# Kernel optimization log

Hardware: AMD Instinct MI355X
Metric: run time of the kernel (lower is better)

Reference implementation:

```python
import jax, jax.numpy as jnp
import numpy as np

EPS = 0.1
P, C, T_MLP, C_MLP, B = 196, 768, 384, 3072, 64


def yat(x, W, b, alpha):
    # x: (..., in), W: (out, in), b: (out,), alpha: (1,)
    dot_nb = jnp.einsum('...i,oi->...o', x, W)          # no-bias dot (shared GEMM)
    dot = dot_nb + b
    w_norm_sq = jnp.sum(W * W, axis=1)                   # (out,)
    x_norm_sq = jnp.sum(x * x, axis=-1, keepdims=True)   # (..., 1)
    dist_sq = w_norm_sq + x_norm_sq - 2.0 * dot_nb
    out_f = W.shape[0]
    scale_base = out_f / np.log(out_f + 1.0)
    scale = jnp.sqrt(jnp.asarray(scale_base, x.dtype)) ** alpha[0]
    return scale * (dot * dot) / (dist_sq + EPS)


def setup_inputs() -> dict:
    key = jax.random.key(0)
    ks = jax.random.split(key, 7)
    x = jax.random.normal(ks[0], (B, P, C), dtype=jnp.float32)
    # token-mixing YAT: in=P, out=T_MLP
    tw = jax.random.normal(ks[1], (T_MLP, P), dtype=jnp.float32) / np.sqrt(P)
    tb = jnp.zeros((T_MLP,), jnp.float32)
    t_alpha = jnp.ones((1,), jnp.float32)
    # token-mixing linear: T_MLP -> P
    w2 = jax.random.uniform(ks[2], (P, T_MLP), jnp.float32, -1, 1) / np.sqrt(T_MLP)
    b2 = jax.random.uniform(ks[3], (P,), jnp.float32, -1, 1) / np.sqrt(T_MLP)
    # channel-mixing YAT: in=C, out=C_MLP
    cw = jax.random.normal(ks[4], (C_MLP, C), dtype=jnp.float32) / np.sqrt(C)
    cb = jnp.zeros((C_MLP,), jnp.float32)
    c_alpha = jnp.ones((1,), jnp.float32)
    # channel-mixing linear: C_MLP -> C
    w4 = jax.random.uniform(ks[5], (C, C_MLP), jnp.float32, -1, 1) / np.sqrt(C_MLP)
    b4 = jax.random.uniform(ks[6], (C,), jnp.float32, -1, 1) / np.sqrt(C_MLP)
    return {"x": x, "tw": tw, "tb": tb, "t_alpha": t_alpha, "w2": w2, "b2": b2,
            "cw": cw, "cb": cb, "c_alpha": c_alpha, "w4": w4, "b4": b4}


def reference(x, tw, tb, t_alpha, w2, b2, cw, cb, c_alpha, w4, b4):
    # Token mixing (operates over patch dim)
    shortcut = x
    xt = jnp.swapaxes(x, 1, 2)                 # (B, C, P)
    h = yat(xt, tw, tb, t_alpha)               # (B, C, T_MLP)
    h = jnp.einsum('bct,pt->bcp', h, w2) + b2  # (B, C, P)
    x = shortcut + jnp.swapaxes(h, 1, 2)
    # Channel mixing (operates over hidden dim)
    shortcut = x
    h = yat(x, cw, cb, c_alpha)                # (B, P, C_MLP)
    h = jnp.einsum('bpm,cm->bpc', h, w4) + b4  # (B, P, C)
    return shortcut + h
```

## Files before the change

kernel.cpp:

```cpp
#include <hip/hip_runtime.h>
#include <hip/hip_bf16.h>
#include <math.h>

#define B_   64
#define P_   196
#define PPAD 224
#define C_   768
#define TM_  384
#define CM_  3072
#define EPSY 0.1f

typedef unsigned short u16;
typedef __attribute__((ext_vector_type(8))) short bf16x8;
typedef __attribute__((ext_vector_type(4))) float f32x4;

__device__ __forceinline__ float bf2f(u16 v) {
    return __uint_as_float(((unsigned int)v) << 16);
}
__device__ __forceinline__ u16 f2bf(float f) {
    unsigned int u = __float_as_uint(f);
    unsigned int rounding = 0x7FFFu + ((u >> 16) & 1u);
    return (u16)((u + rounding) >> 16);
}

__device__ __forceinline__ void gl_lds16(const u16* g, u16* l) {
    __builtin_amdgcn_global_load_lds(
        (const __attribute__((address_space(1))) unsigned int*)g,
        (__attribute__((address_space(3))) unsigned int*)l,
        16, 0, 0);
}


__global__ __launch_bounds__(256) void k_prep_xT(const float* __restrict__ x,
                                                 u16* __restrict__ xT,
                                                 float* __restrict__ xn1) {
    __shared__ u16 tile[32][33];
    __shared__ float colsum[32];
    const int b = blockIdx.z, p0 = blockIdx.x * 32, c0 = blockIdx.y * 32;
    const int tx = threadIdx.x & 31, ty = threadIdx.x >> 5;
    if (threadIdx.x < 32) colsum[threadIdx.x] = 0.f;
    const float* xb = x + (size_t)b * P_ * C_;
    float s = 0.f;
    #pragma unroll
    for (int r = 0; r < 4; ++r) {
        int p = p0 + ty + r * 8;
        float v = (p < P_) ? xb[(size_t)p * C_ + c0 + tx] : 0.f;
        u16 h = f2bf(v);
        tile[ty + r * 8][tx] = h;
        float vb = bf2f(h);
        s = fmaf(vb, vb, s);
    }
    __syncthreads();
    u16* dst = xT + ((size_t)b * C_ + c0) * PPAD + p0;
    #pragma unroll
    for (int r = 0; r < 4; ++r) {
        int cl = ty + r * 8;
        dst[(size_t)cl * PPAD + tx] = tile[tx][cl];
    }
    atomicAdd(&colsum[tx], s);
    __syncthreads();
    if (threadIdx.x < 32)
        atomicAdd(&xn1[(size_t)b * C_ + c0 + threadIdx.x], colsum[threadIdx.x]);
}

__device__ __forceinline__ void pad_norm_body(const float* in, u16* outb, float* norm,
                                              int rows, int inlen, int outlen,
                                              int bid, int tid) {
    int wave = (bid * 256 + tid) >> 6;
    int lane = tid & 63;
    if (wave >= rows) return;
    const float* src = in + (size_t)wave * inlen;
    u16* dst = outb + (size_t)wave * outlen;
    float s = 0.f;
    for (int i = lane; i < outlen; i += 64) {
        float v = (i < inlen) ? src[i] : 0.f;
        u16 h = f2bf(v);
        dst[i] = h;
        float vv = bf2f(h);
        s = fmaf(vv, vv, s);
    }
    #pragma unroll
    for (int off = 32; off > 0; off >>= 1) s += __shfl_down(s, off, 64);
    if (lane == 0) norm[wave] = s;
}

__global__ __launch_bounds__(256) void k_prep_weights(
    const float* __restrict__ tw, u16* __restrict__ twb, float* __restrict__ twn,
    const float* __restrict__ cw, u16* __restrict__ cwb, float* __restrict__ cwn,
    const float* __restrict__ w2, u16* __restrict__ w2b,
    const float* __restrict__ w4, u16* __restrict__ w4b) {
    int bid = blockIdx.x, tid = threadIdx.x;
    if (bid < 96) {
        pad_norm_body(tw, twb, twn, TM_, P_, PPAD, bid, tid);
    } else if (bid < 864) {
        pad_norm_body(cw, cwb, cwn, CM_, C_, C_, bid - 96, tid);
    } else if (bid < 1248) {
        int idx = (bid - 864) * 256 + tid;
        int row = idx / TM_;
        w2b[idx] = (row < P_) ? f2bf(w2[(size_t)row * TM_ + (idx % TM_)]) : (u16)0;
    } else {
        int idx = (bid - 1248) * 256 + tid;
        float4 v = ((const float4*)w4)[idx];
        ushort4 o;
        o.x = f2bf(v.x); o.y = f2bf(v.y); o.z = f2bf(v.z); o.w = f2bf(v.w);
        ((ushort4*)w4b)[idx] = o;
    }
}

__device__ __forceinline__ void mfma_mainloop(
    const u16* __restrict__ A, const u16* __restrict__ B,
    int lda, int ldb, int kiters,
    f32x4 (&acc)[4][4], u16* As, u16* Bs) {
    const int t = threadIdx.x;
    const int w = t >> 6, l = t & 63;
    const int quad = l >> 4, l15 = l & 15;
    const int row0 = t >> 2, kc = (t & 3) * 8;
    const int row1 = 64 + row0;

    gl_lds16(A + (size_t)row0 * lda + kc, As + w * 512);
    gl_lds16(A + (size_t)row1 * lda + kc, As + 2048 + w * 512);
    gl_lds16(B + (size_t)row0 * ldb + kc, Bs + w * 512);
    gl_lds16(B + (size_t)row1 * ldb + kc, Bs + 2048 + w * 512);
    __syncthreads();

    int cur = 0;
    for (int it = 0; it < kiters; ++it) {
        if (it + 1 < kiters) {
            const int k0 = (it + 1) * 32;
            const int nb = (cur ^ 1) * 4096;
            gl_lds16(A + (size_t)row0 * lda + k0 + kc, As + nb + w * 512);
            gl_lds16(A + (size_t)row1 * lda + k0 + kc, As + nb + 2048 + w * 512);
            gl_lds16(B + (size_t)row0 * ldb + k0 + kc, Bs + nb + w * 512);
            gl_lds16(B + (size_t)row1 * ldb + k0 + kc, Bs + nb + 2048 + w * 512);
        }
        const u16* Aw = As + cur * 4096 + (w >> 1) * 2048;
        const u16* Bw = Bs + cur * 4096 + (w & 1) * 2048;
        bf16x8 af[4], bfr[4];
        #pragma unroll
        for (int i = 0; i < 4; ++i)
            af[i] = *(const bf16x8*)(Aw + ((i * 16 + l15) * 32 + quad * 8));
        #pragma unroll
        for (int j = 0; j < 4; ++j)
            bfr[j] = *(const bf16x8*)(Bw + ((j * 16 + l15) * 32 + quad * 8));
        #pragma unroll
        for (int i = 0; i < 4; ++i)
            #pragma unroll
            for (int j = 0; j < 4; ++j)
                acc[i][j] = __builtin_amdgcn_mfma_f32_16x16x32_bf16(af[i], bfr[j], acc[i][j], 0, 0, 0);
        __syncthreads();
        cur ^= 1;
    }
}

#define MFMA_CORE(AP, BP, LDA, LDB, KITERS)                              \
    __shared__ u16 As[2 * 128 * 32];                                     \
    __shared__ u16 Bs[2 * 128 * 32];                                     \
    const int t = threadIdx.x;                                           \
    const int wid = t >> 6, lane = t & 63;                               \
    const int quad = lane >> 4, l15 = lane & 15;                         \
    f32x4 acc[4][4];                                                     \
    _Pragma("unroll")                                                    \
    for (int i = 0; i < 4; ++i)                                          \
        _Pragma("unroll")                                                \
        for (int j = 0; j < 4; ++j) acc[i][j] = (f32x4){0.f,0.f,0.f,0.f};\
    mfma_mainloop(AP, BP, LDA, LDB, KITERS, acc, As, Bs);                \
    const int rbase = m0 + (wid >> 1) * 64;                              \
    const int cbase = n0 + (wid & 1) * 64;

__global__ __launch_bounds__(256) void k1_token_yat(
    const u16* __restrict__ xT, const u16* __restrict__ twb,
    const float* __restrict__ tb, const float* __restrict__ twn,
    const float* __restrict__ xn1, const float* __restrict__ alpha, float sb,
    u16* __restrict__ h1) {
    const int m0 = (blockIdx.x + blockIdx.y * 8) * 128;
    const int n0 = blockIdx.z * 128;
    MFMA_CORE(xT + (size_t)m0 * PPAD, twb + (size_t)n0 * PPAD, PPAD, PPAD, PPAD / 32)
    float scale = powf(sqrtf(sb), alpha[0]);
    #pragma unroll
    for (int i = 0; i < 4; ++i) {
        #pragma unroll
        for (int j = 0; j < 4; ++j) {
            int col = cbase + j * 16 + l15;
            float bn = tb[col], wnn = twn[col];
            #pragma unroll
            for (int reg = 0; reg < 4; ++reg) {
                int row = rbase + i * 16 + quad * 4 + reg;
                float dnb = acc[i][j][reg];
                float dot = dnb + bn;
                float dist = wnn + xn1[row] - 2.f * dnb;
                h1[(size_t)row * TM_ + col] = f2bf(scale * dot * dot / (dist + EPSY));
            }
        }
    }
}

__global__ __launch_bounds__(256) void k3_chan_yat(
    const u16* __restrict__ x1b, const u16* __restrict__ cwb,
    const float* __restrict__ cb, const float* __restrict__ cwn,
    const float* __restrict__ xn2, const float* __restrict__ alpha, float sb,
    u16* __restrict__ h3) {
    const int mt = blockIdx.x + blockIdx.y * 8;
    if (mt >= B_ * P_ / 128) return;
    const int m0 = mt * 128;
    const int n0 = blockIdx.z * 128;
    MFMA_CORE(x1b + (size_t)m0 * C_, cwb + (size_t)n0 * C_, C_, C_, C_ / 32)
    float scale = powf(sqrtf(sb), alpha[0]);
    #pragma unroll
    for (int i = 0; i < 4; ++i) {
        #pragma unroll
        for (int j = 0; j < 4; ++j) {
            int col = cbase + j * 16 + l15;
            float bn = cb[col], wnn = cwn[col];
            #pragma unroll
            for (int reg = 0; reg < 4; ++reg) {
                int row = rbase + i * 16 + quad * 4 + reg;
                float dnb = acc[i][j][reg];
                float dot = dnb + bn;
                float dist = wnn + xn2[row] - 2.f * dnb;
                h3[(size_t)row * CM_ + col] = f2bf(scale * dot * dot / (dist + EPSY));
            }
        }
    }
}

__global__ __launch_bounds__(256) void k2_token_out(
    const u16* __restrict__ w2b, const u16* __restrict__ h1,
    const float* __restrict__ b2, const float* __restrict__ x,
    float* __restrict__ xn2, u16* __restrict__ x1b) {
    const int m0 = blockIdx.x * 128, n0 = blockIdx.y * 128;
    const u16* Bz = h1 + (size_t)blockIdx.z * C_ * TM_;
    MFMA_CORE(w2b + (size_t)m0 * TM_, Bz + (size_t)n0 * TM_, TM_, TM_, TM_ / 32)
    const float* rz = x + (size_t)blockIdx.z * P_ * C_;
    u16* oz = x1b + (size_t)blockIdx.z * P_ * C_;
    float* xrow = xn2 + (size_t)blockIdx.z * P_;
    #pragma unroll
    for (int i = 0; i < 4; ++i) {
        #pragma unroll
        for (int reg = 0; reg < 4; ++reg) {
            int row = rbase + i * 16 + quad * 4 + reg;
            if (row < P_) {
                float bm = b2[row];
                float s = 0.f;
                #pragma unroll
                for (int j = 0; j < 4; ++j) {
                    int col = cbase + j * 16 + l15;
                    float v = acc[i][j][reg] + bm + rz[(size_t)row * C_ + col];
                    u16 h = f2bf(v);
                    oz[(size_t)row * C_ + col] = h;
                    float vb = bf2f(h);
                    s = fmaf(vb, vb, s);
                }
                s += __shfl_xor(s, 1, 64);
                s += __shfl_xor(s, 2, 64);
                s += __shfl_xor(s, 4, 64);
                s += __shfl_xor(s, 8, 64);
                if (l15 == 0) atomicAdd(&xrow[row], s);
            }
        }
    }
}

__global__ __launch_bounds__(256) void k4_split(
    const u16* __restrict__ h3, const u16* __restrict__ w4b,
    u16* __restrict__ pbuf, int KK) {
    const int mt = blockIdx.x + blockIdx.y * 8;
    if (mt >= B_ * P_ / 128) return;
    const int m0 = mt * 128;
    const int nz = blockIdx.z;
    const int n0 = (nz % (C_ / 128)) * 128;
    const int ks = nz / (C_ / 128);
    const int kbase = ks * KK;
    MFMA_CORE(h3 + (size_t)m0 * CM_ + kbase, w4b + (size_t)n0 * CM_ + kbase,
              CM_, CM_, KK / 32)
    u16* dst = pbuf + (size_t)ks * ((size_t)B_ * P_ * C_);
    #pragma unroll
    for (int i = 0; i < 4; ++i) {
        #pragma unroll
        for (int j = 0; j < 4; ++j) {
            int col = cbase + j * 16 + l15;
            #pragma unroll
            for (int reg = 0; reg < 4; ++reg) {
                int row = rbase + i * 16 + quad * 4 + reg;
                dst[(size_t)row * C_ + col] = f2bf(acc[i][j][reg]);
            }
        }
    }
}

template <int NS>
__global__ __launch_bounds__(256) void k4_reduce(
    float* __restrict__ outp, const u16* __restrict__ pbuf,
    const u16* __restrict__ x1b, const float* __restrict__ b4) {
    int idx = blockIdx.x * 256 + threadIdx.x;
    int c = (idx * 4) % C_;
    ushort4 r = ((const ushort4*)x1b)[idx];
    float4 o;
    o.x = bf2f(r.x) + b4[c + 0];
    o.y = bf2f(r.y) + b4[c + 1];
    o.z = bf2f(r.z) + b4[c + 2];
    o.w = bf2f(r.w) + b4[c + 3];
    const size_t stride4 = (size_t)B_ * P_ * C_ / 4;
    #pragma unroll
    for (int s = 0; s < NS; ++s) {
        ushort4 p = ((const ushort4*)pbuf)[idx + s * stride4];
        o.x += bf2f(p.x); o.y += bf2f(p.y); o.z += bf2f(p.z); o.w += bf2f(p.w);
    }
    ((float4*)outp)[idx] = o;
}

__global__ __launch_bounds__(256) void gemm_k4_fb(
    const u16* __restrict__ A, const u16* __restrict__ Bmat,
    const float* __restrict__ biasN, const u16* __restrict__ resB,
    float* __restrict__ Fout) {
    __shared__ u16 As[128 * 32];
    __shared__ u16 Bs[64 * 32];
    const int t = threadIdx.x;
    const int wid = t >> 6, lane = t & 63;
    const int quad = lane >> 4, l15 = lane & 15;
    const int m0 = blockIdx.x * 128, n0 = blockIdx.y * 64;
    f32x4 acc[4][2];
    #pragma unroll
    for (int i = 0; i < 4; ++i)
        #pragma unroll
        for (int j = 0; j < 2; ++j) acc[i][j] = (f32x4){0.f, 0.f, 0.f, 0.f};
    const u16* Aw = As + (wid >> 1) * (64 * 32);
    const u16* Bw = Bs + (wid & 1) * (32 * 32);
    const int arow = t >> 2, akc = (t & 3) * 8;
    for (int k0 = 0; k0 < CM_; k0 += 32) {
        gl_lds16(A + (size_t)(m0 + arow) * CM_ + k0 + akc,      As + wid * 512);
        gl_lds16(A + (size_t)(m0 + 64 + arow) * CM_ + k0 + akc, As + 2048 + wid * 512);
        gl_lds16(Bmat + (size_t)(n0 + arow) * CM_ + k0 + akc,   Bs + wid * 512);
        __syncthreads();
        bf16x8 af[4], bfr[2];
        #pragma unroll
        for (int i = 0; i < 4; ++i)
            af[i] = *(const bf16x8*)(Aw + ((i * 16 + l15) * 32 + quad * 8));
        #pragma unroll
        for (int j = 0; j < 2; ++j)
            bfr[j] = *(const bf16x8*)(Bw + ((j * 16 + l15) * 32 + quad * 8));
        #pragma unroll
        for (int i = 0; i < 4; ++i)
            #pragma unroll
            for (int j = 0; j < 2; ++j)
                acc[i][j] = __builtin_amdgcn_mfma_f32_16x16x32_bf16(af[i], bfr[j], acc[i][j], 0, 0, 0);
        __syncthreads();
    }
    const int rbase = m0 + (wid >> 1) * 64;
    const int cbase = n0 + (wid & 1) * 32;
    #pragma unroll
    for (int i = 0; i < 4; ++i) {
        #pragma unroll
        for (int j = 0; j < 2; ++j) {
            int col = cbase + j * 16 + l15;
            float bn = biasN[col];
            #pragma unroll
            for (int reg = 0; reg < 4; ++reg) {
                int row = rbase + i * 16 + quad * 4 + reg;
                float v = acc[i][j][reg] + bn + bf2f(resB[(size_t)row * C_ + col]);
                Fout[(size_t)row * C_ + col] = v;
            }
        }
    }
}

extern "C" void kernel_launch(void* const* d_in, const int* in_sizes, int n_in,
                              void* d_out, int out_size, void* d_ws, size_t ws_size,
                              hipStream_t stream) {
    const float* x  = (const float*)d_in[0];
    const float* tw = (const float*)d_in[1];
    const float* tb = (const float*)d_in[2];
    const float* ta = (const float*)d_in[3];
    const float* w2 = (const float*)d_in[4];
    const float* b2 = (const float*)d_in[5];
    const float* cw = (const float*)d_in[6];
    const float* cb = (const float*)d_in[7];
    const float* ca = (const float*)d_in[8];
    const float* w4 = (const float*)d_in[9];
    const float* b4 = (const float*)d_in[10];
    float* out = (float*)d_out;

    char* ws = (char*)d_ws;
    u16* h1 = (u16*)ws;
    u16* xT = (u16*)(ws + 37748736);
    u16* h3 = (u16*)ws;
    size_t off = 77070336;
    u16* x1b = (u16*)(ws + off); off += (size_t)B_ * P_ * C_ * 2;
    u16* twb = (u16*)(ws + off); off += (size_t)TM_ * PPAD * 2;
    u16* w2b = (u16*)(ws + off); off += (size_t)256 * TM_ * 2;
    u16* cwb = (u16*)(ws + off); off += (size_t)CM_ * C_ * 2;
    u16* w4b = (u16*)(ws + off); off += (size_t)C_ * CM_ * 2;
    float* xn1 = (float*)(ws + off); off += (size_t)B_ * C_ * 4;
    float* xn2 = (float*)(ws + off); off += (size_t)B_ * P_ * 4;
    float* twn = (float*)(ws + off); off += (size_t)TM_ * 4;
    float* cwn = (float*)(ws + off); off += (size_t)CM_ * 4;
    u16* pbuf = (u16*)(ws + off);
    const size_t psz = (size_t)B_ * P_ * C_ * 2;

    int nsplit = 1;
    if (ws_size >= off + 4 * psz)      nsplit = 4;
    else if (ws_size >= off + 2 * psz) nsplit = 2;

    const float SBT = (float)TM_ / logf((float)TM_ + 1.0f);
    const float SBC = (float)CM_ / logf((float)CM_ + 1.0f);

    hipMemsetAsync(xn1, 0, (size_t)(B_ * C_ + B_ * P_) * 4, stream);
    k_prep_weights<<<3552, 256, 0, stream>>>(tw, twb, twn, cw, cwb, cwn,
                                             w2, w2b, w4, w4b);
    k_prep_xT<<<dim3(PPAD / 32, C_ / 32, B_), 256, 0, stream>>>(x, xT, xn1);

    k1_token_yat<<<dim3(8, 48, 3), 256, 0, stream>>>(
        xT, twb, tb, twn, xn1, ta, SBT, h1);

    k2_token_out<<<dim3(2, C_ / 128, B_), 256, 0, stream>>>(
        w2b, h1, b2, x, xn2, x1b);

    k3_chan_yat<<<dim3(8, 13, 24), 256, 0, stream>>>(
        x1b, cwb, cb, cwn, xn2, ca, SBC, h3);

    if (nsplit > 1) {
        k4_split<<<dim3(8, 13, (C_ / 128) * nsplit), 256, 0, stream>>>(
            h3, w4b, pbuf, CM_ / nsplit);
        int n4 = B_ * P_ * C_ / 4;
        if (nsplit == 4)
            k4_reduce<4><<<(n4 + 255) / 256, 256, 0, stream>>>(out, pbuf, x1b, b4);
        else
            k4_reduce<2><<<(n4 + 255) / 256, 256, 0, stream>>>(out, pbuf, x1b, b4);
    } else {
        gemm_k4_fb<<<dim3(B_ * P_ / 128, C_ / 64), 256, 0, stream>>>(
            h3, w4b, b4, x1b, out);
    }
}
```

Measured before the change: 405.3 us.

## Prefetch two K-stages ahead in MFMA mainloop with fine-grained waitcnt and barriers

Restructures the shared GEMM mainloop so global-to-LDS loads run two iterations ahead, issued right after the current tile's fragments are read into registers. The single __syncthreads is replaced by explicit vmcnt/lgkmcnt waits and raw s_barrier calls. s_setprio is raised around the MFMA block. The aim is to hide global load latency behind MFMA work, at the cost of relying on hand-counted vmcnt values being correct for the LDS reuse pattern.

Result: faster. 385.5 us (-4.9%).

```diff
diff --git a/kernel.cpp b/kernel.cpp
--- a/kernel.cpp
+++ b/kernel.cpp
@@ -115,24 +115,38 @@
     const int w = t >> 6, l = t & 63;
     const int quad = l >> 4, l15 = l & 15;
     const int row0 = t >> 2, kc = (t & 3) * 8;
-    const int row1 = 64 + row0;
-
-    gl_lds16(A + (size_t)row0 * lda + kc, As + w * 512);
-    gl_lds16(A + (size_t)row1 * lda + kc, As + 2048 + w * 512);
-    gl_lds16(B + (size_t)row0 * ldb + kc, Bs + w * 512);
-    gl_lds16(B + (size_t)row1 * ldb + kc, Bs + 2048 + w * 512);
-    __syncthreads();
+
+    const u16* pa0 = A + (size_t)row0 * lda + kc;
+    const u16* pa1 = A + (size_t)(64 + row0) * lda + kc;
+    const u16* pb0 = B + (size_t)row0 * ldb + kc;
+    const u16* pb1 = B + (size_t)(64 + row0) * ldb + kc;
+
+    u16* ldsA0 = As + w * 512;
+    u16* ldsA1 = As + 2048 + w * 512;
+    u16* ldsB0 = Bs + w * 512;
+    u16* ldsB1 = Bs + 2048 + w * 512;
+
+#define STAGE_(bsel, koff)                          \
+    do {                                            \
+        const int nb_ = (bsel) * 4096;              \
+        gl_lds16(pa0 + (koff), ldsA0 + nb_);        \
+        gl_lds16(pa1 + (koff), ldsA1 + nb_);        \
+        gl_lds16(pb0 + (koff), ldsB0 + nb_);        \
+        gl_lds16(pb1 + (koff), ldsB1 + nb_);        \
+    } while (0)
+
+    STAGE_(0, 0);
+    if (kiters > 1) {
+        STAGE_(1, 32);
+        asm volatile("s_waitcnt vmcnt(4)" ::: "memory");
+    } else {
+        asm volatile("s_waitcnt vmcnt(0)" ::: "memory");
+    }
+    __builtin_amdgcn_s_barrier();
 
     int cur = 0;
+    int koff = 64;
     for (int it = 0; it < kiters; ++it) {
-        if (it + 1 < kiters) {
-            const int k0 = (it + 1) * 32;
-            const int nb = (cur ^ 1) * 4096;
-            gl_lds16(A + (size_t)row0 * lda + k0 + kc, As + nb + w * 512);
-            gl_lds16(A + (size_t)row1 * lda + k0 + kc, As + nb + 2048 + w * 512);
-            gl_lds16(B + (size_t)row0 * ldb + k0 + kc, Bs + nb + w * 512);
-            gl_lds16(B + (size_t)row1 * ldb + k0 + kc, Bs + nb + 2048 + w * 512);
-        }
         const u16* Aw = As + cur * 4096 + (w >> 1) * 2048;
         const u16* Bw = Bs + cur * 4096 + (w & 1) * 2048;
         bf16x8 af[4], bfr[4];
@@ -142,14 +156,26 @@
         #pragma unroll
         for (int j = 0; j < 4; ++j)
             bfr[j] = *(const bf16x8*)(Bw + ((j * 16 + l15) * 32 + quad * 8));
+        asm volatile("s_waitcnt lgkmcnt(0)" ::: "memory");
+        __builtin_amdgcn_sched_barrier(0);
+        __builtin_amdgcn_s_barrier();
+        const bool more2 = (it + 2 < kiters);
+        if (more2) { STAGE_(cur, koff); koff += 32; }
+        __builtin_amdgcn_s_setprio(1);
         #pragma unroll
         for (int i = 0; i < 4; ++i)
             #pragma unroll
             for (int j = 0; j < 4; ++j)
                 acc[i][j] = __builtin_amdgcn_mfma_f32_16x16x32_bf16(af[i], bfr[j], acc[i][j], 0, 0, 0);
-        __syncthreads();
+        __builtin_amdgcn_s_setprio(0);
+        if (it + 1 < kiters) {
+            if (more2) asm volatile("s_waitcnt vmcnt(4)" ::: "memory");
+            else       asm volatile("s_waitcnt vmcnt(0)" ::: "memory");
+            __builtin_amdgcn_s_barrier();
+        }
         cur ^= 1;
     }
+#undef STAGE_
 }
 
 #define MFMA_CORE(AP, BP, LDA, LDB, KITERS)                              \
```
